# Optimization experiments

Measured on AMD Instinct MI355X. Metric: run time of the kernel, lower is better.

## Reference

```python
import jax, jax.numpy as jnp
import numpy as np

B, S, H, NH = 1, 4096, 1024, 16
DH = H // NH


def setup_inputs() -> dict:
    key = jax.random.key(0)
    ks = jax.random.split(key, 9)
    sc = 0.02
    return {
        "queries": jax.random.normal(ks[0], (B, S, H), jnp.float32),
        "keys": jax.random.normal(ks[1], (B, S, H), jnp.float32),
        "values": jax.random.normal(ks[2], (B, S, H), jnp.float32),
        "Wq_w": jax.random.normal(ks[3], (H, H), jnp.float32) * sc,
        "Wq_b": jax.random.normal(ks[4], (H,), jnp.float32) * sc,
        "Wk_w": jax.random.normal(ks[5], (H, H), jnp.float32) * sc,
        "Wk_b": jax.random.normal(ks[6], (H,), jnp.float32) * sc,
        "Wv_w": jax.random.normal(ks[7], (H, H), jnp.float32) * sc,
        "Wv_b": jax.random.normal(ks[8], (H,), jnp.float32) * sc,
    }


def _split_heads(x):
    # torch.chunk(x, NH, dim=-1) then stack(dim=1) == reshape + transpose
    b, s, h = x.shape
    return jnp.transpose(x.reshape(b, s, NH, DH), (0, 2, 1, 3))  # [B,NH,S,DH]


def reference(queries, keys, values, Wq_w, Wq_b, Wk_w, Wk_b, Wv_w, Wv_b):
    q = jax.nn.relu(queries @ Wq_w.T + Wq_b)
    k = jax.nn.relu(keys @ Wk_w.T + Wk_b)
    v = jax.nn.relu(values @ Wv_w.T + Wv_b)
    qh, kh, vh = _split_heads(q), _split_heads(k), _split_heads(v)
    score = jnp.einsum("bhsd,bhtd->bhst", qh, kh) / jnp.sqrt(jnp.float32(DH))
    attn = jax.nn.softmax(score, axis=-1)
    a = jnp.einsum("bhst,bhtd->bhsd", attn, vh)  # [B,NH,S,DH]
    # faithful to torch: permute(0,1,3,2) -> [B,NH,DH,S], then reshape to (B,S,H)
    a = jnp.transpose(a, (0, 1, 3, 2)).reshape(q.shape[0], q.shape[1], q.shape[2])
    return a + queries
```

## Files before the change

kernel.cpp:

```cpp
#include <hip/hip_runtime.h>
#include <stdint.h>


#define SEQ 4096
#define HID 1024
#define NHEAD 16
#define DHEAD 64

typedef __attribute__((ext_vector_type(8))) short short8_t;
typedef __attribute__((ext_vector_type(4))) float f32x4;
typedef __attribute__((ext_vector_type(16))) float f32x16;
typedef __attribute__((ext_vector_type(2))) unsigned int u32x2;

#define WS_QB   0u
#define WS_KB   4194304u
#define WS_VB   8388608u
#define WS_WQ   12582912u
#define WS_QO   15728640u
#define WS_KO   19922944u
#define WS_VT   24117248u

__device__ __forceinline__ unsigned short f2bf(float f) {
  union { float f; unsigned int u; } x; x.f = f;
  unsigned int u = x.u;
  return (unsigned short)((u + 0x7FFFu + ((u >> 16) & 1u)) >> 16);
}

__device__ __forceinline__ float fexp2(float x) {
#if __has_builtin(__builtin_amdgcn_exp2f)
  return __builtin_amdgcn_exp2f(x);
#else
  float r; asm("v_exp_f32 %0, %1" : "=v"(r) : "v"(x)); return r;
#endif
}

__device__ __forceinline__ unsigned int pk2(float a, float b) {
  unsigned int r;
  asm("v_cvt_pk_bf16_f32 %0, %1, %2" : "=v"(r) : "v"(a), "v"(b));
  return r;
}

__device__ __forceinline__ void pl32swap(unsigned int& a, unsigned int& b) {
  asm("v_permlane32_swap_b32 %0, %1" : "+v"(a), "+v"(b));
}

__device__ __forceinline__ void gll16(const void* g, void* l) {
  __builtin_amdgcn_global_load_lds(
      (const __attribute__((address_space(1))) void*)g,
      (__attribute__((address_space(3))) void*)l, 16, 0, 0);
}

__global__ void __launch_bounds__(256) prep_convert(
    const float* __restrict__ qin, const float* __restrict__ kin,
    const float* __restrict__ vin, const float* __restrict__ wq,
    const float* __restrict__ wk, const float* __restrict__ wv,
    unsigned short* __restrict__ ws) {
  const int total = 3932160;
  for (int i = blockIdx.x * blockDim.x + threadIdx.x; i < total;
       i += gridDim.x * blockDim.x) {
    const float* src; unsigned short* dst; int off;
    if (i < 3145728) {
      int which = i >> 20;
      off = (i & 1048575) << 2;
      src = which == 0 ? qin : (which == 1 ? kin : vin);
      dst = ws + which * 4194304u;
    } else {
      int j = i - 3145728;
      int which = j >> 18;
      off = (j & 262143) << 2;
      src = which == 0 ? wq : (which == 1 ? wk : wv);
      dst = ws + WS_WQ + which * 1048576u;
    }
    float4 f = *(const float4*)(src + off);
    u32x2 p;
    p.x = f2bf(f.x) | ((unsigned int)f2bf(f.y) << 16);
    p.y = f2bf(f.z) | ((unsigned int)f2bf(f.w) << 16);
    *(u32x2*)(dst + off) = p;
  }
}

__global__ void __launch_bounds__(256) qkv_gemm(
    unsigned short* __restrict__ ws, const float* __restrict__ bq,
    const float* __restrict__ bk, const float* __restrict__ bv) {
  __shared__ alignas(16) unsigned short lA[128 * 32];
  __shared__ alignas(16) unsigned short lB[128 * 32];
  const int z = blockIdx.z;
  const unsigned short* A = ws + z * 4194304u;
  const unsigned short* W = ws + WS_WQ + z * 1048576u;
  const float* bias = z == 0 ? bq : (z == 1 ? bk : bv);
  const int tid = threadIdx.x;
  const int lane = tid & 63;
  const int wid = tid >> 6;
  const int wr = wid >> 1, wc = wid & 1;
  const int bm = blockIdx.y, bn = blockIdx.x;
  const int l15 = lane & 15, l4 = lane >> 4;

  f32x4 acc[4][4];
#pragma unroll
  for (int m = 0; m < 4; ++m)
#pragma unroll
    for (int n = 0; n < 4; ++n) acc[m][n] = {0.f, 0.f, 0.f, 0.f};

  const int srow = lane >> 2;
  const int scs = lane & 3;

  for (int kt = 0; kt < 1024; kt += 32) {
    __syncthreads();
#pragma unroll
    for (int c = 0; c < 2; ++c) {
      const int row = c * 64 + wid * 16 + srow;
      const int ch = scs ^ ((row >> 1) & 3);
      gll16(A + (size_t)(bm * 128 + row) * 1024 + kt + ch * 8,
            (char*)lA + c * 4096 + wid * 1024);
      gll16(W + (size_t)(bn * 128 + row) * 1024 + kt + ch * 8,
            (char*)lB + c * 4096 + wid * 1024);
    }
    __syncthreads();
    short8_t af[4], bf[4];
#pragma unroll
    for (int m = 0; m < 4; ++m) {
      const int row = wr * 64 + m * 16 + l15;
      const int ch = l4 ^ ((row >> 1) & 3);
      af[m] = *(const short8_t*)(lA + row * 32 + ch * 8);
    }
#pragma unroll
    for (int n = 0; n < 4; ++n) {
      const int row = wc * 64 + n * 16 + l15;
      const int ch = l4 ^ ((row >> 1) & 3);
      bf[n] = *(const short8_t*)(lB + row * 32 + ch * 8);
    }
#pragma unroll
    for (int m = 0; m < 4; ++m)
#pragma unroll
      for (int n = 0; n < 4; ++n)
        acc[m][n] = __builtin_amdgcn_mfma_f32_16x16x32_bf16(af[m], bf[n],
                                                            acc[m][n], 0, 0, 0);
  }

  const int row0 = bm * 128 + wr * 64;
  const int col0 = bn * 128 + wc * 64;
  if (z < 2) {
    const float scl = (z == 1) ? 0.18033688011112042f : 1.0f;
    unsigned short* o = ws + WS_QO + z * 4194304u;
#pragma unroll
    for (int n = 0; n < 4; ++n) {
      const int col = col0 + n * 16 + l15;
      const float bb = bias[col];
#pragma unroll
      for (int m = 0; m < 4; ++m)
#pragma unroll
        for (int j = 0; j < 4; ++j) {
          const int row = row0 + m * 16 + l4 * 4 + j;
          o[(size_t)row * 1024 + col] = f2bf(fmaxf(acc[m][n][j] + bb, 0.f) * scl);
        }
    }
  } else {
    unsigned short* vt = ws + WS_VT;
#pragma unroll
    for (int n = 0; n < 4; ++n) {
      const int col = col0 + n * 16 + l15;
      const float bb = bias[col];
      const int nh = col >> 6, d = col & 63;
#pragma unroll
      for (int m = 0; m < 4; ++m) {
        const int t0 = row0 + m * 16 + l4 * 4;
        u32x2 p;
        p.x = f2bf(fmaxf(acc[m][n][0] + bb, 0.f)) |
              ((unsigned int)f2bf(fmaxf(acc[m][n][1] + bb, 0.f)) << 16);
        p.y = f2bf(fmaxf(acc[m][n][2] + bb, 0.f)) |
              ((unsigned int)f2bf(fmaxf(acc[m][n][3] + bb, 0.f)) << 16);
        *(u32x2*)(vt + (size_t)nh * 262144 + (size_t)d * 4096 + t0) = p;
      }
    }
  }
}

__global__ void __launch_bounds__(256, 4) attn_fwd(
    const unsigned short* __restrict__ ws, const float* __restrict__ qin,
    float* __restrict__ out) {
  __shared__ alignas(16) char smem[33792];
  unsigned short* lKb = (unsigned short*)smem;
  unsigned short* lVb = (unsigned short*)(smem + 16384);
  float* fO = (float*)smem;
  float* fRs = (float*)(smem + 33280);

  const unsigned short* qo = ws + WS_QO;
  const char* koB = (const char*)(ws + WS_KO);
  const char* vtB = (const char*)(ws + WS_VT);
  const int nh = blockIdx.y;
  const int qb0 = blockIdx.x * 64;
  const int tid = threadIdx.x, lane = tid & 63, wid = tid >> 6;
  const int l31 = lane & 31, l5 = lane >> 5;
  const int qw = wid >> 1, tw = wid & 1;
  const int sq = qb0 + qw * 32 + l31;

  const int stt = tid >> 3;
  const int sch = tid & 7;
  unsigned kboff[2], vboff[2];
#pragma unroll
  for (int r = 0; r < 2; ++r) {
    const int tt = r * 32 + stt;
    const int ch = sch ^ (tt & 7);
    kboff[r] = (unsigned)(tt * 1024 + nh * 64 + ch * 8) * 2u;
    vboff[r] = (unsigned)(nh * 262144 + tt * 4096 + ch * 8) * 2u;
  }

  short8_t qf[4];
#pragma unroll
  for (int kcd = 0; kcd < 4; ++kcd)
    qf[kcd] = *(const short8_t*)(qo + (size_t)sq * 1024 + nh * 64 +
                                 kcd * 16 + l5 * 8);

  union { unsigned int u[4]; short8_t v; } ou;
  {
    const unsigned int ov = (l31 == 0) ? 0x3F803F80u : 0u;
    ou.u[0] = ov; ou.u[1] = ov; ou.u[2] = ov; ou.u[3] = ov;
  }
  const short8_t ones = ou.v;

  int kofl[4];
  {
    const int row = tw * 32 + l31;
#pragma unroll
    for (int kcd = 0; kcd < 4; ++kcd)
      kofl[kcd] = row * 128 + (((kcd * 2 + l5) ^ (row & 7)) * 16);
  }
  int vofl[2][2];
#pragma unroll
  for (int n = 0; n < 2; ++n) {
    const int row = n * 32 + l31;
#pragma unroll
    for (int kc = 0; kc < 2; ++kc)
      vofl[n][kc] = row * 128 + (((tw * 4 + kc * 2 + l5) ^ (row & 7)) * 16);
  }

  f32x16 aco0, aco1, acl;
#pragma unroll
  for (int r = 0; r < 16; ++r) { aco0[r] = 0.f; aco1[r] = 0.f; acl[r] = 0.f; }

#define STAGE(buf, kvb)                                                        \
  {                                                                            \
    const unsigned kvbK = (unsigned)(kvb) * 2048u;                             \
    const unsigned kvbV = (unsigned)(kvb) * 2u;                                \
    _Pragma("unroll") for (int r = 0; r < 2; ++r) {                            \
      gll16(koB + (kboff[r] + kvbK),                                           \
            (char*)lKb + (buf) * 8192 + r * 4096 + wid * 1024);                \
      gll16(vtB + (vboff[r] + kvbV),                                           \
            (char*)lVb + (buf) * 8192 + r * 4096 + wid * 1024);                \
    }                                                                          \
  }

  STAGE(0, 0);
  __syncthreads();
  int cur = 0;

  for (int kv = 0; kv < 4096; kv += 64) {
    if (kv + 64 < 4096) STAGE(cur ^ 1, kv + 64);
    const char* lKc = (const char*)lKb + cur * 8192;
    const char* lVc = (const char*)lVb + cur * 8192;

    f32x16 acs;
#pragma unroll
    for (int r = 0; r < 16; ++r) acs[r] = 0.f;
    __builtin_amdgcn_s_setprio(1);
#pragma unroll
    for (int kcd = 0; kcd < 4; ++kcd) {
      const short8_t kfr = *(const short8_t*)(lKc + kofl[kcd]);
      acs = __builtin_amdgcn_mfma_f32_32x32x16_bf16(kfr, qf[kcd], acs, 0, 0, 0);
    }
    __builtin_amdgcn_s_setprio(0);

#pragma unroll
    for (int r = 0; r < 16; ++r) acs[r] = fexp2(acs[r]);

    unsigned int w0 = pk2(acs[0], acs[1]),   w1 = pk2(acs[2], acs[3]);
    unsigned int w2 = pk2(acs[4], acs[5]),   w3 = pk2(acs[6], acs[7]);
    unsigned int w4 = pk2(acs[8], acs[9]),   w5 = pk2(acs[10], acs[11]);
    unsigned int w6 = pk2(acs[12], acs[13]), w7 = pk2(acs[14], acs[15]);
    pl32swap(w0, w2);
    pl32swap(w1, w3);
    pl32swap(w4, w6);
    pl32swap(w5, w7);
    union { unsigned int u[4]; short8_t v; } pa0, pa1;
    pa0.u[0] = w0; pa0.u[1] = w1; pa0.u[2] = w2; pa0.u[3] = w3;
    pa1.u[0] = w4; pa1.u[1] = w5; pa1.u[2] = w6; pa1.u[3] = w7;

    __builtin_amdgcn_s_setprio(1);
    {
      const short8_t vf00 = *(const short8_t*)(lVc + vofl[0][0]);
      const short8_t vf10 = *(const short8_t*)(lVc + vofl[1][0]);
      aco0 = __builtin_amdgcn_mfma_f32_32x32x16_bf16(pa0.v, vf00, aco0, 0, 0, 0);
      aco1 = __builtin_amdgcn_mfma_f32_32x32x16_bf16(pa0.v, vf10, aco1, 0, 0, 0);
      acl = __builtin_amdgcn_mfma_f32_32x32x16_bf16(pa0.v, ones, acl, 0, 0, 0);
      const short8_t vf01 = *(const short8_t*)(lVc + vofl[0][1]);
      const short8_t vf11 = *(const short8_t*)(lVc + vofl[1][1]);
      aco0 = __builtin_amdgcn_mfma_f32_32x32x16_bf16(pa1.v, vf01, aco0, 0, 0, 0);
      aco1 = __builtin_amdgcn_mfma_f32_32x32x16_bf16(pa1.v, vf11, aco1, 0, 0, 0);
      acl = __builtin_amdgcn_mfma_f32_32x32x16_bf16(pa1.v, ones, acl, 0, 0, 0);
    }
    __builtin_amdgcn_s_setprio(0);

    __syncthreads();
    cur ^= 1;
  }

  {
    float* myO = fO + tw * 64 * 65;
#pragma unroll
    for (int r = 0; r < 16; ++r) {
      const int sl = (r & 3) + 8 * (r >> 2) + 4 * l5;
      const int s = qw * 32 + sl;
      myO[(l31) * 65 + s] = aco0[r];
      myO[(l31 + 32) * 65 + s] = aco1[r];
    }
    if (l31 == 0) {
#pragma unroll
      for (int r = 0; r < 16; ++r) {
        const int sl = (r & 3) + 8 * (r >> 2) + 4 * l5;
        fRs[tw * 64 + qw * 32 + sl] = acl[r];
      }
    }
  }
  __syncthreads();

  {
    const int s = tid & 63;
    const int sg = qb0 + s;
    const float inv = 1.f / (fRs[s] + fRs[64 + s]);
    const int scol = sg & 1023, srow = sg >> 10;
#pragma unroll
    for (int i = 0; i < 16; ++i) {
      const int d = (tid >> 6) * 16 + i;
      const float v = fO[d * 65 + s] + fO[64 * 65 + d * 65 + s];
      const int idx = (nh * 256 + d * 4 + srow) * 1024 + scol;
      out[idx] = qin[idx] + v * inv;
    }
  }
#undef STAGE
}

extern "C" void kernel_launch(void* const* d_in, const int* in_sizes, int n_in,
                              void* d_out, int out_size, void* d_ws,
                              size_t ws_size, hipStream_t stream) {
  const float* qin = (const float*)d_in[0];
  const float* kin = (const float*)d_in[1];
  const float* vin = (const float*)d_in[2];
  const float* wq = (const float*)d_in[3];
  const float* bq = (const float*)d_in[4];
  const float* wk = (const float*)d_in[5];
  const float* bk = (const float*)d_in[6];
  const float* wv = (const float*)d_in[7];
  const float* bv = (const float*)d_in[8];
  unsigned short* ws = (unsigned short*)d_ws;
  float* out = (float*)d_out;

  prep_convert<<<dim3(8192), dim3(256), 0, stream>>>(qin, kin, vin, wq, wk, wv, ws);
  qkv_gemm<<<dim3(8, 32, 3), dim3(256), 0, stream>>>(ws, bq, bk, bv);
  attn_fwd<<<dim3(64, 16), dim3(256), 0, stream>>>(ws, qin, out);
}
```

Measured before the change: 148.4 us.

## Double query rows per attention block and remap qkv_gemm block order

```diff
diff --git a/kernel.cpp b/kernel.cpp
--- a/kernel.cpp
+++ b/kernel.cpp
@@ -49,6 +49,24 @@
       (const __attribute__((address_space(1))) void*)g,
       (__attribute__((address_space(3))) void*)l, 16, 0, 0);
 }
+
+__device__ __forceinline__ void packP(const f32x16& a, short8_t& p0,
+                                      short8_t& p1) {
+  unsigned int w0 = pk2(a[0], a[1]),   w1 = pk2(a[2], a[3]);
+  unsigned int w2 = pk2(a[4], a[5]),   w3 = pk2(a[6], a[7]);
+  unsigned int w4 = pk2(a[8], a[9]),   w5 = pk2(a[10], a[11]);
+  unsigned int w6 = pk2(a[12], a[13]), w7 = pk2(a[14], a[15]);
+  pl32swap(w0, w2);
+  pl32swap(w1, w3);
+  pl32swap(w4, w6);
+  pl32swap(w5, w7);
+  union { unsigned int u[4]; short8_t v; } q0, q1;
+  q0.u[0] = w0; q0.u[1] = w1; q0.u[2] = w2; q0.u[3] = w3;
+  q1.u[0] = w4; q1.u[1] = w5; q1.u[2] = w6; q1.u[3] = w7;
+  p0 = q0.v; p1 = q1.v;
+}
+
+#define MFMA32(a, b, c) __builtin_amdgcn_mfma_f32_32x32x16_bf16(a, b, c, 0, 0, 0)
 
 __global__ void __launch_bounds__(256) prep_convert(
     const float* __restrict__ qin, const float* __restrict__ kin,
@@ -92,7 +110,9 @@
   const int lane = tid & 63;
   const int wid = tid >> 6;
   const int wr = wid >> 1, wc = wid & 1;
-  const int bm = blockIdx.y, bn = blockIdx.x;
+  const int lin = blockIdx.y * 8 + blockIdx.x;
+  const int nid = (lin & 7) * 32 + (lin >> 3);
+  const int bm = nid >> 3, bn = nid & 7;
   const int l15 = lane & 15, l4 = lane >> 4;
 
   f32x4 acc[4][4];
@@ -175,7 +195,7 @@
   }
 }
 
-__global__ void __launch_bounds__(256, 4) attn_fwd(
+__global__ void __launch_bounds__(256, 2) attn_fwd(
     const unsigned short* __restrict__ ws, const float* __restrict__ qin,
     float* __restrict__ out) {
   __shared__ alignas(16) char smem[33792];
@@ -188,11 +208,11 @@
   const char* koB = (const char*)(ws + WS_KO);
   const char* vtB = (const char*)(ws + WS_VT);
   const int nh = blockIdx.y;
-  const int qb0 = blockIdx.x * 64;
+  const int qb0 = blockIdx.x * 128;
   const int tid = threadIdx.x, lane = tid & 63, wid = tid >> 6;
   const int l31 = lane & 31, l5 = lane >> 5;
-  const int qw = wid >> 1, tw = wid & 1;
-  const int sq = qb0 + qw * 32 + l31;
+  const int qg = wid >> 1, tw = wid & 1;
+  const int sqg = qb0 + qg * 64;
 
   const int stt = tid >> 3;
   const int sch = tid & 7;
@@ -205,11 +225,13 @@
     vboff[r] = (unsigned)(nh * 262144 + tt * 4096 + ch * 8) * 2u;
   }
 
-  short8_t qf[4];
-#pragma unroll
-  for (int kcd = 0; kcd < 4; ++kcd)
-    qf[kcd] = *(const short8_t*)(qo + (size_t)sq * 1024 + nh * 64 +
-                                 kcd * 16 + l5 * 8);
+  short8_t qf[2][4];
+#pragma unroll
+  for (int cg = 0; cg < 2; ++cg)
+#pragma unroll
+    for (int kcd = 0; kcd < 4; ++kcd)
+      qf[cg][kcd] = *(const short8_t*)(qo + (size_t)(sqg + cg * 32 + l31) * 1024 +
+                                       nh * 64 + kcd * 16 + l5 * 8);
 
   union { unsigned int u[4]; short8_t v; } ou;
   {
@@ -234,9 +256,11 @@
       vofl[n][kc] = row * 128 + (((tw * 4 + kc * 2 + l5) ^ (row & 7)) * 16);
   }
 
-  f32x16 aco0, aco1, acl;
-#pragma unroll
-  for (int r = 0; r < 16; ++r) { aco0[r] = 0.f; aco1[r] = 0.f; acl[r] = 0.f; }
+  f32x16 zro;
+#pragma unroll
+  for (int r = 0; r < 16; ++r) zro[r] = 0.f;
+  f32x16 aco00 = zro, aco01 = zro, aco10 = zro, aco11 = zro;
+  f32x16 acl0 = zro, acl1 = zro;
 
 #define STAGE(buf, kvb)                                                        \
   {                                                                            \
@@ -259,81 +283,90 @@
     const char* lKc = (const char*)lKb + cur * 8192;
     const char* lVc = (const char*)lVb + cur * 8192;
 
-    f32x16 acs;
-#pragma unroll
-    for (int r = 0; r < 16; ++r) acs[r] = 0.f;
+    short8_t kfr[4];
+#pragma unroll
+    for (int kcd = 0; kcd < 4; ++kcd)
+      kfr[kcd] = *(const short8_t*)(lKc + kofl[kcd]);
+
     __builtin_amdgcn_s_setprio(1);
-#pragma unroll
-    for (int kcd = 0; kcd < 4; ++kcd) {
-      const short8_t kfr = *(const short8_t*)(lKc + kofl[kcd]);
-      acs = __builtin_amdgcn_mfma_f32_32x32x16_bf16(kfr, qf[kcd], acs, 0, 0, 0);
+    f32x16 acs0 = MFMA32(kfr[0], qf[0][0], zro);
+    f32x16 acs1 = MFMA32(kfr[0], qf[1][0], zro);
+#pragma unroll
+    for (int kcd = 1; kcd < 4; ++kcd) {
+      acs0 = MFMA32(kfr[kcd], qf[0][kcd], acs0);
+      acs1 = MFMA32(kfr[kcd], qf[1][kcd], acs1);
     }
     __builtin_amdgcn_s_setprio(0);
 
 #pragma unroll
-    for (int r = 0; r < 16; ++r) acs[r] = fexp2(acs[r]);
-
-    unsigned int w0 = pk2(acs[0], acs[1]),   w1 = pk2(acs[2], acs[3]);
-    unsigned int w2 = pk2(acs[4], acs[5]),   w3 = pk2(acs[6], acs[7]);
-    unsigned int w4 = pk2(acs[8], acs[9]),   w5 = pk2(acs[10], acs[11]);
-    unsigned int w6 = pk2(acs[12], acs[13]), w7 = pk2(acs[14], acs[15]);
-    pl32swap(w0, w2);
-    pl32swap(w1, w3);
-    pl32swap(w4, w6);
-    pl32swap(w5, w7);
-    union { unsigned int u[4]; short8_t v; } pa0, pa1;
-    pa0.u[0] = w0; pa0.u[1] = w1; pa0.u[2] = w2; pa0.u[3] = w3;
-    pa1.u[0] = w4; pa1.u[1] = w5; pa1.u[2] = w6; pa1.u[3] = w7;
+    for (int r = 0; r < 16; ++r) {
+      acs0[r] = fexp2(acs0[r]);
+      acs1[r] = fexp2(acs1[r]);
+    }
+
+    short8_t pa00, pa01, pa10, pa11;
+    packP(acs0, pa00, pa01);
+    packP(acs1, pa10, pa11);
+
+    const short8_t vf00 = *(const short8_t*)(lVc + vofl[0][0]);
+    const short8_t vf10 = *(const short8_t*)(lVc + vofl[1][0]);
+    const short8_t vf01 = *(const short8_t*)(lVc + vofl[0][1]);
+    const short8_t vf11 = *(const short8_t*)(lVc + vofl[1][1]);
 
     __builtin_amdgcn_s_setprio(1);
-    {
-      const short8_t vf00 = *(const short8_t*)(lVc + vofl[0][0]);
-      const short8_t vf10 = *(const short8_t*)(lVc + vofl[1][0]);
-      aco0 = __builtin_amdgcn_mfma_f32_32x32x16_bf16(pa0.v, vf00, aco0, 0, 0, 0);
-      aco1 = __builtin_amdgcn_mfma_f32_32x32x16_bf16(pa0.v, vf10, aco1, 0, 0, 0);
-      acl = __builtin_amdgcn_mfma_f32_32x32x16_bf16(pa0.v, ones, acl, 0, 0, 0);
-      const short8_t vf01 = *(const short8_t*)(lVc + vofl[0][1]);
-      const short8_t vf11 = *(const short8_t*)(lVc + vofl[1][1]);
-      aco0 = __builtin_amdgcn_mfma_f32_32x32x16_bf16(pa1.v, vf01, aco0, 0, 0, 0);
-      aco1 = __builtin_amdgcn_mfma_f32_32x32x16_bf16(pa1.v, vf11, aco1, 0, 0, 0);
-      acl = __builtin_amdgcn_mfma_f32_32x32x16_bf16(pa1.v, ones, acl, 0, 0, 0);
-    }
+    aco00 = MFMA32(pa00, vf00, aco00);
+    aco10 = MFMA32(pa10, vf00, aco10);
+    aco01 = MFMA32(pa00, vf10, aco01);
+    aco11 = MFMA32(pa10, vf10, aco11);
+    acl0 = MFMA32(pa00, ones, acl0);
+    acl1 = MFMA32(pa10, ones, acl1);
+    aco00 = MFMA32(pa01, vf01, aco00);
+    aco10 = MFMA32(pa11, vf01, aco10);
+    aco01 = MFMA32(pa01, vf11, aco01);
+    aco11 = MFMA32(pa11, vf11, aco11);
+    acl0 = MFMA32(pa01, ones, acl0);
+    acl1 = MFMA32(pa11, ones, acl1);
     __builtin_amdgcn_s_setprio(0);
 
     __syncthreads();
     cur ^= 1;
   }
 
-  {
-    float* myO = fO + tw * 64 * 65;
-#pragma unroll
-    for (int r = 0; r < 16; ++r) {
-      const int sl = (r & 3) + 8 * (r >> 2) + 4 * l5;
-      const int s = qw * 32 + sl;
-      myO[(l31) * 65 + s] = aco0[r];
-      myO[(l31 + 32) * 65 + s] = aco1[r];
-    }
-    if (l31 == 0) {
+#pragma unroll
+  for (int p = 0; p < 2; ++p) {
+    if (p) __syncthreads();
+    if (qg == p) {
+      float* myO = fO + tw * 4160;
 #pragma unroll
       for (int r = 0; r < 16; ++r) {
         const int sl = (r & 3) + 8 * (r >> 2) + 4 * l5;
-        fRs[tw * 64 + qw * 32 + sl] = acl[r];
+        myO[l31 * 65 + sl] = aco00[r];
+        myO[(l31 + 32) * 65 + sl] = aco01[r];
+        myO[l31 * 65 + 32 + sl] = aco10[r];
+        myO[(l31 + 32) * 65 + 32 + sl] = aco11[r];
       }
-    }
-  }
-  __syncthreads();
-
-  {
-    const int s = tid & 63;
-    const int sg = qb0 + s;
-    const float inv = 1.f / (fRs[s] + fRs[64 + s]);
-    const int scol = sg & 1023, srow = sg >> 10;
-#pragma unroll
-    for (int i = 0; i < 16; ++i) {
-      const int d = (tid >> 6) * 16 + i;
-      const float v = fO[d * 65 + s] + fO[64 * 65 + d * 65 + s];
-      const int idx = (nh * 256 + d * 4 + srow) * 1024 + scol;
-      out[idx] = qin[idx] + v * inv;
+      if (l31 == 0) {
+#pragma unroll
+        for (int r = 0; r < 16; ++r) {
+          const int sl = (r & 3) + 8 * (r >> 2) + 4 * l5;
+          fRs[tw * 64 + sl] = acl0[r];
+          fRs[tw * 64 + 32 + sl] = acl1[r];
+        }
+      }
+    }
+    __syncthreads();
+    {
+      const int s = tid & 63;
+      const int sg = qb0 + p * 64 + s;
+      const float inv = 1.f / (fRs[s] + fRs[64 + s]);
+      const int scol = sg & 1023, srow = sg >> 10;
+#pragma unroll
+      for (int i = 0; i < 16; ++i) {
+        const int d = (tid >> 6) * 16 + i;
+        const float v = fO[d * 65 + s] + fO[4160 + d * 65 + s];
+        const int idx = (nh * 256 + d * 4 + srow) * 1024 + scol;
+        out[idx] = qin[idx] + v * inv;
+      }
     }
   }
 #undef STAGE
@@ -356,5 +389,5 @@
 
   prep_convert<<<dim3(8192), dim3(256), 0, stream>>>(qin, kin, vin, wq, wk, wv, ws);
   qkv_gemm<<<dim3(8, 32, 3), dim3(256), 0, stream>>>(ws, bq, bk, bv);
-  attn_fwd<<<dim3(64, 16), dim3(256), 0, stream>>>(ws, qin, out);
-}
+  attn_fwd<<<dim3(32, 16), dim3(256), 0, stream>>>(ws, qin, out);
+}
```

New measurement: 136.6 us. 1.09x faster.
